# Kernel tuning notes

Hardware: AMD Instinct MI355X
Metric: run time of the kernel (lower is better)

The kernel has to match this reference:

```python
import jax, jax.numpy as jnp
import numpy as np

NUM_FUTURE = 4  # num_future_time_steps module constant


def _wmean(x, src, dst, ew, n):
    # Weighted mean aggregation over incoming edges (PyG SAGEConv aggr='mean'
    # with edge-weighted messages). x: [N,F] or [T,N,F].
    if x.ndim == 2:
        msg = x[src] * ew[:, None]                          # [E,F]
        agg = jax.ops.segment_sum(msg, dst, num_segments=n)  # [N,F]
    else:
        msg = x[:, src, :] * ew[None, :, None]              # [T,E,F]
        agg = jax.ops.segment_sum(jnp.moveaxis(msg, 1, 0), dst, num_segments=n)
        agg = jnp.moveaxis(agg, 0, 1)                       # [T,N,F]
    deg = jax.ops.segment_sum(jnp.ones_like(ew), dst, num_segments=n)
    return agg / jnp.clip(deg, 1.0)[:, None]


def _sage(x, src, dst, ew, Wr, Wroot, b, n):
    # WeightedSAGEConv: lin_rel(weighted-mean of neighbors) + lin_root(x)
    return _wmean(x, src, dst, ew, n) @ Wr + x @ Wroot + b


def _glstm(xseq, src, dst, ew, Wr, Wroot, b, h0, c0, n):
    # Graph LSTM: all four gates are WeightedSAGEConv([x_t, h]) ; the gate
    # convs share one gather/scatter (linear in agg), weights stacked to 4H.
    def step(carry, xt):
        h, c = carry
        inp = jnp.concatenate([xt, h], axis=-1)             # [N,2H]
        gates = _wmean(inp, src, dst, ew, n) @ Wr + inp @ Wroot + b  # [N,4H]
        i, f, g, o = jnp.split(gates, 4, axis=-1)
        c = jax.nn.sigmoid(f) * c + jax.nn.sigmoid(i) * jnp.tanh(g)
        h = jax.nn.sigmoid(o) * jnp.tanh(c)
        return (h, c), h
    (h, c), hs = jax.lax.scan(step, (h0, c0), xseq)
    return hs, c  # hs: [T,N,H]


def setup_inputs():
    T, N, E = 12, 20000, 400000
    F, H, O = 32, 64, 8
    key = jax.random.key(0)
    ks = jax.random.split(key, 12)
    nrm = lambda k, shp, fan: jax.random.normal(k, shp, dtype=jnp.float32) / np.float32(np.sqrt(fan))
    return {
        "x": jax.random.normal(ks[0], (T, N, F), dtype=jnp.float32),
        "edge_index": jax.random.randint(ks[1], (2, E), 0, N, dtype=jnp.int32),
        "edge_attr": jax.random.uniform(ks[2], (E,), dtype=jnp.float32),
        "sage_Wr": nrm(ks[3], (F, H), F),
        "sage_Wroot": nrm(ks[4], (F, H), F),
        "sage_b": jnp.zeros((H,), jnp.float32),
        "lstm1_Wr": nrm(ks[5], (2 * H, 4 * H), 2 * H),
        "lstm1_Wroot": nrm(ks[6], (2 * H, 4 * H), 2 * H),
        "lstm1_b": jnp.zeros((4 * H,), jnp.float32),
        "lstm2_Wr": nrm(ks[7], (2 * H, 4 * H), 2 * H),
        "lstm2_Wroot": nrm(ks[8], (2 * H, 4 * H), 2 * H),
        "lstm2_b": jnp.zeros((4 * H,), jnp.float32),
        "W_out": nrm(ks[9], (2 * H, O), 2 * H),
        "b_out": jnp.zeros((O,), jnp.float32),
    }


def reference(x, edge_index, edge_attr, sage_Wr, sage_Wroot, sage_b,
              lstm1_Wr, lstm1_Wroot, lstm1_b, lstm2_Wr, lstm2_Wroot, lstm2_b,
              W_out, b_out):
    src, dst = edge_index[0], edge_index[1]
    N = x.shape[1]
    H = sage_Wr.shape[1]
    emb = _sage(x, src, dst, edge_attr, sage_Wr, sage_Wroot, sage_b, N)  # [T,N,H]
    xr = jax.nn.relu(emb)  # dropout = identity (eval mode)
    h0 = jnp.zeros((N, H), x.dtype)
    c0 = jnp.zeros((N, H), x.dtype)
    h1, c1 = _glstm(xr, src, dst, edge_attr, lstm1_Wr, lstm1_Wroot, lstm1_b, h0, c0, N)
    h2, c2 = _glstm(xr, src, dst, edge_attr, lstm2_Wr, lstm2_Wroot, lstm2_b, h1[-1], c1, N)
    xs = jnp.concatenate([xr, h2], axis=-1)              # skip connection, [T,N,2H]
    out = xs[-NUM_FUTURE:] @ W_out + b_out               # [4,N,O]
    return out, c2, emb
```

## Files before the change

### kernel.cpp

```cpp
#include <hip/hip_runtime.h>
#include <math.h>

#define TT 12
#define FF 32
#define HH 64
#define OO 8
#define GG 256
#define NF 4
#define BR 16

typedef __bf16 bf16x8 __attribute__((ext_vector_type(8)));
typedef float  f32x4  __attribute__((ext_vector_type(4)));

__device__ __forceinline__ float sigmoidf_(float x){ return 1.f/(1.f+expf(-x)); }
__device__ __forceinline__ unsigned short f2bf(float f){
  unsigned int u = __float_as_uint(f);
  u += 0x7FFFu + ((u >> 16) & 1u);
  return (unsigned short)(u >> 16);
}
__device__ __forceinline__ float bf2f(unsigned short b){
  return __uint_as_float(((unsigned int)b) << 16);
}

__global__ void hist_kernel(const int* __restrict__ dst, int* __restrict__ cnt, int E){
  int e = blockIdx.x*blockDim.x + threadIdx.x;
  if (e < E) atomicAdd(&cnt[dst[e]], 1);
}

__global__ __launch_bounds__(1024) void scan_kernel(const int* __restrict__ cnt,
                                                    int* __restrict__ ptr,
                                                    float* __restrict__ invd, int N){
  __shared__ int buf[1024];
  __shared__ int carry;
  if (threadIdx.x == 0) carry = 0;
  __syncthreads();
  for (int base = 0; base < N; base += 1024){
    int i = base + threadIdx.x;
    int v = (i < N) ? cnt[i] : 0;
    buf[threadIdx.x] = v;
    __syncthreads();
    for (int off = 1; off < 1024; off <<= 1){
      int t = (threadIdx.x >= off) ? buf[threadIdx.x - off] : 0;
      __syncthreads();
      buf[threadIdx.x] += t;
      __syncthreads();
    }
    int incl = buf[threadIdx.x];
    if (i < N){
      ptr[i] = carry + incl - v;
      invd[i] = 1.f / fmaxf((float)v, 1.f);
    }
    __syncthreads();
    if (threadIdx.x == 1023){
      carry += incl;
      if (base + 1024 >= N) ptr[N] = carry;
    }
    __syncthreads();
  }
}

__global__ void fill_kernel(const int* __restrict__ src, const int* __restrict__ dst,
                            const float* __restrict__ ew, const int* __restrict__ ptr,
                            int* __restrict__ fill, int2* __restrict__ csr_sw, int E){
  int e = blockIdx.x*blockDim.x + threadIdx.x;
  if (e >= E) return;
  int d = dst[e];
  int pos = ptr[d] + atomicAdd(&fill[d], 1);
  int2 m; m.x = src[e]; m.y = __float_as_int(ew[e]);
  csr_sw[pos] = m;
}

__global__ void xpose_conv(const float* __restrict__ in, unsigned short* __restrict__ out,
                           int N){
  int idx = blockIdx.x*blockDim.x + threadIdx.x;
  if (idx >= TT*N*FF) return;
  int f = idx & (FF-1);
  int rem = idx >> 5;
  int t = rem % TT, n = rem / TT;
  out[idx] = f2bf(in[(size_t)t*N*FF + (size_t)n*FF + f]);
}

__global__ void pack_wfrag(const float* __restrict__ Wr, const float* __restrict__ Wroot,
                           unsigned short* __restrict__ Wfrag){
  int idx = blockIdx.x*256 + threadIdx.x;
  if (idx >= 16*8*64*8) return;
  int e  = idx & 7;
  int l  = (idx >> 3) & 63;
  int ks = (idx >> 9) & 7;
  int jt = idx >> 12;
  int k = ks*32 + (l>>4)*8 + e;
  int j = jt*16 + (l&15);
  float v = (k < 128) ? Wr[(size_t)k*GG + j] : Wroot[(size_t)(k-128)*GG + j];
  Wfrag[idx] = f2bf(v);
}

__global__ void pack_sfrag(const float* __restrict__ Wr, const float* __restrict__ Wroot,
                           unsigned short* __restrict__ Sfrag){
  int idx = blockIdx.x*256 + threadIdx.x;
  if (idx >= 4*2*64*8) return;
  int e  = idx & 7;
  int l  = (idx >> 3) & 63;
  int ks = (idx >> 9) & 1;
  int jt = idx >> 10;
  int k = ks*32 + (l>>4)*8 + e;
  int j = jt*16 + (l&15);
  float v = (k < 32) ? Wr[(size_t)k*HH + j] : Wroot[(size_t)(k-32)*HH + j];
  Sfrag[idx] = f2bf(v);
}

__global__ __launch_bounds__(256) void sage_gather(
    const unsigned short* __restrict__ xb, const int* __restrict__ ptr,
    const int2* __restrict__ csr_sw,
    const float* __restrict__ invd, unsigned short* __restrict__ aggb, int N){
  int wave = threadIdx.x >> 6, lane = threadIdx.x & 63;
  int f = lane & 31, tp = lane >> 5;
  int n = blockIdx.x*4 + wave;
  if (n >= N) return;
  int beg = ptr[n], end = ptr[n+1];
  float id = invd[n];
  float acc[TT/2];
  #pragma unroll
  for (int th = 0; th < TT/2; ++th) acc[th] = 0.f;
  int e = beg;
  for (; e+2 <= end; e += 2){
    int2 m0 = csr_sw[e], m1 = csr_sw[e+1];
    const unsigned short* p0 = xb + (size_t)m0.x*TT*FF + tp*FF + f;
    const unsigned short* p1 = xb + (size_t)m1.x*TT*FF + tp*FF + f;
    float w0 = __int_as_float(m0.y), w1 = __int_as_float(m1.y);
    #pragma unroll
    for (int th = 0; th < TT/2; ++th)
      acc[th] += bf2f(p0[2*th*FF])*w0 + bf2f(p1[2*th*FF])*w1;
  }
  for (; e < end; ++e){
    int2 m = csr_sw[e];
    const unsigned short* p = xb + (size_t)m.x*TT*FF + tp*FF + f;
    float wv = __int_as_float(m.y);
    #pragma unroll
    for (int th = 0; th < TT/2; ++th)
      acc[th] += bf2f(p[2*th*FF])*wv;
  }
  #pragma unroll
  for (int th = 0; th < TT/2; ++th)
    aggb[(size_t)n*TT*FF + (2*th+tp)*FF + f] = f2bf(acc[th] * id);
}

__global__ __launch_bounds__(256) void sage_mfma(
    const unsigned short* __restrict__ aggb, const unsigned short* __restrict__ xb,
    const unsigned short* __restrict__ Sfrag, const float* __restrict__ bias,
    float* __restrict__ emb, unsigned short* __restrict__ xrb, int N, int Mrows){
  int tid = threadIdx.x, wave = tid >> 6, lane = tid & 63;
  int rbase = blockIdx.x*64 + wave*16;
  if (rbase >= Mrows) return;
  int l15 = lane & 15, l4 = lane >> 4;
  int row = rbase + l15;
  bf16x8 af0 = *(const bf16x8*)&aggb[(size_t)row*FF + l4*8];
  bf16x8 af1 = *(const bf16x8*)&xb  [(size_t)row*FF + l4*8];
  f32x4 acc[4];
  #pragma unroll
  for (int jt = 0; jt < 4; ++jt){
    float bv = bias[jt*16 + l15];
    acc[jt][0]=bv; acc[jt][1]=bv; acc[jt][2]=bv; acc[jt][3]=bv;
  }
  #pragma unroll
  for (int jt = 0; jt < 4; ++jt){
    bf16x8 b0 = *(const bf16x8*)&Sfrag[(size_t)(((jt*2+0)*64) + lane) * 8];
    bf16x8 b1 = *(const bf16x8*)&Sfrag[(size_t)(((jt*2+1)*64) + lane) * 8];
    acc[jt] = __builtin_amdgcn_mfma_f32_16x16x32_bf16(af0, b0, acc[jt], 0, 0, 0);
    acc[jt] = __builtin_amdgcn_mfma_f32_16x16x32_bf16(af1, b1, acc[jt], 0, 0, 0);
  }
  #pragma unroll
  for (int jt = 0; jt < 4; ++jt){
    int col = jt*16 + l15;
    #pragma unroll
    for (int i = 0; i < 4; ++i){
      int ro = rbase + l4*4 + i;
      int t = ro % TT, n = ro / TT;
      float v = acc[jt][i];
      emb[(size_t)t*N*HH + (size_t)n*HH + col] = v;
      xrb[(size_t)ro*HH + col] = f2bf(fmaxf(v, 0.f));
    }
  }
}

__global__ __launch_bounds__(256) void xr_gather(
    const unsigned short* __restrict__ xrb, const int* __restrict__ ptr,
    const int2* __restrict__ csr_sw,
    const float* __restrict__ invd, unsigned short* __restrict__ xr_aggb, int N){
  int wave = threadIdx.x >> 6, lane = threadIdx.x & 63;
  int n = blockIdx.x*4 + wave;
  if (n >= N) return;
  int beg = ptr[n], end = ptr[n+1];
  float id = invd[n];
  float acc[TT];
  #pragma unroll
  for (int t = 0; t < TT; ++t) acc[t] = 0.f;
  int e = beg;
  for (; e+2 <= end; e += 2){
    int2 m0 = csr_sw[e], m1 = csr_sw[e+1];
    const unsigned short* p0 = xrb + (size_t)m0.x*TT*HH + lane;
    const unsigned short* p1 = xrb + (size_t)m1.x*TT*HH + lane;
    float w0 = __int_as_float(m0.y), w1 = __int_as_float(m1.y);
    #pragma unroll
    for (int t = 0; t < TT; ++t)
      acc[t] += bf2f(p0[t*HH])*w0 + bf2f(p1[t*HH])*w1;
  }
  for (; e < end; ++e){
    int2 m = csr_sw[e];
    const unsigned short* p = xrb + (size_t)m.x*TT*HH + lane;
    float wv = __int_as_float(m.y);
    #pragma unroll
    for (int t = 0; t < TT; ++t)
      acc[t] += bf2f(p[t*HH])*wv;
  }
  #pragma unroll
  for (int t = 0; t < TT; ++t)
    xr_aggb[(size_t)n*TT*HH + t*HH + lane] = f2bf(acc[t] * id);
}

__global__ __launch_bounds__(1024) void lstm_mfma(
    const unsigned short* __restrict__ xrb_t, const unsigned short* __restrict__ xraggb_t,
    const unsigned short* __restrict__ h_prev, unsigned short* __restrict__ h_next,
    float* __restrict__ c, const float* __restrict__ invd,
    const int* __restrict__ ptr, const int2* __restrict__ csr_sw,
    const unsigned short* __restrict__ Wfrag, const float* __restrict__ bias,
    unsigned short* __restrict__ h2_store, int N){
  __shared__ __align__(16) unsigned short Albuf[BR][264];
  __shared__ float gbuf[BR][260];
  int tid = threadIdx.x, wave = tid >> 6, lane = tid & 63;
  int base = blockIdx.x * BR;
  int n = base + wave;

  if (n < N){
    float id = invd[n];
    int beg = ptr[n], end = ptr[n+1];
    float a0=0.f,a1=0.f,a2=0.f,a3=0.f,a4=0.f,a5=0.f,a6=0.f,a7=0.f;
    int e = beg;
    for (; e+8 <= end; e += 8){
      int2 m0=csr_sw[e+0], m1=csr_sw[e+1], m2=csr_sw[e+2], m3=csr_sw[e+3];
      int2 m4=csr_sw[e+4], m5=csr_sw[e+5], m6=csr_sw[e+6], m7=csr_sw[e+7];
      a0 += bf2f(h_prev[(size_t)m0.x*HH+lane])*__int_as_float(m0.y);
      a1 += bf2f(h_prev[(size_t)m1.x*HH+lane])*__int_as_float(m1.y);
      a2 += bf2f(h_prev[(size_t)m2.x*HH+lane])*__int_as_float(m2.y);
      a3 += bf2f(h_prev[(size_t)m3.x*HH+lane])*__int_as_float(m3.y);
      a4 += bf2f(h_prev[(size_t)m4.x*HH+lane])*__int_as_float(m4.y);
      a5 += bf2f(h_prev[(size_t)m5.x*HH+lane])*__int_as_float(m5.y);
      a6 += bf2f(h_prev[(size_t)m6.x*HH+lane])*__int_as_float(m6.y);
      a7 += bf2f(h_prev[(size_t)m7.x*HH+lane])*__int_as_float(m7.y);
    }
    for (; e < end; ++e){
      int2 m = csr_sw[e];
      a0 += bf2f(h_prev[(size_t)m.x*HH+lane])*__int_as_float(m.y);
    }
    float hag = (((a0+a1)+(a2+a3))+((a4+a5)+(a6+a7))) * id;
    Albuf[wave][    lane] = xraggb_t[(size_t)n*TT*HH + lane];
    Albuf[wave][ 64+lane] = f2bf(hag);
    Albuf[wave][128+lane] = xrb_t [(size_t)n*TT*HH + lane];
    Albuf[wave][192+lane] = h_prev[(size_t)n*HH + lane];
  } else {
    Albuf[wave][lane] = Albuf[wave][64+lane] = Albuf[wave][128+lane] = Albuf[wave][192+lane] = 0;
  }
  __syncthreads();

  int l15 = lane & 15, l4 = lane >> 4;
  int jt = wave;
  f32x4 acc;
  {
    float bv = bias[jt*16 + l15];
    acc[0]=bv; acc[1]=bv; acc[2]=bv; acc[3]=bv;
  }
  #pragma unroll
  for (int ks = 0; ks < 8; ++ks){
    bf16x8 af = *(const bf16x8*)&Albuf[l15][ks*32 + l4*8];
    bf16x8 bf = *(const bf16x8*)&Wfrag[(size_t)(((jt*8 + ks)*64) + lane) * 8];
    acc = __builtin_amdgcn_mfma_f32_16x16x32_bf16(af, bf, acc, 0, 0, 0);
  }
  {
    int col = jt*16 + l15;
    #pragma unroll
    for (int i = 0; i < 4; ++i)
      gbuf[l4*4 + i][col] = acc[i];
  }
  __syncthreads();

  if (n < N){
    int r = wave;
    float gi = gbuf[r][lane], gf = gbuf[r][64+lane], gg2 = gbuf[r][128+lane], go = gbuf[r][192+lane];
    float cn = sigmoidf_(gf)*c[(size_t)n*HH+lane] + sigmoidf_(gi)*tanhf(gg2);
    float hn = sigmoidf_(go)*tanhf(cn);
    c[(size_t)n*HH+lane] = cn;
    unsigned short hb = f2bf(hn);
    h_next[(size_t)n*HH+lane] = hb;
    if (h2_store) h2_store[(size_t)n*HH+lane] = hb;
  }
}

__global__ void out_gemm(const unsigned short* __restrict__ xrb, const unsigned short* __restrict__ h2s,
                         const float* __restrict__ Wout, const float* __restrict__ bout,
                         float* __restrict__ out, int N){
  int idx = blockIdx.x*blockDim.x + threadIdx.x;
  if (idx >= NF*N*OO) return;
  int o = idx & (OO-1);
  int row = idx >> 3;
  int tt = row / N, n = row % N;
  const unsigned short* xv = xrb + ((size_t)n*TT + (TT-NF) + tt)*HH;
  const unsigned short* hv = h2s + (size_t)row*HH;
  float acc = bout[o];
  #pragma unroll
  for (int k = 0; k < HH; ++k)
    acc += bf2f(xv[k])*Wout[k*OO+o] + bf2f(hv[k])*Wout[(HH+k)*OO+o];
  out[idx] = acc;
}

__global__ void copyk(const float* __restrict__ s, float* __restrict__ d, int n){
  int i = blockIdx.x*blockDim.x + threadIdx.x;
  if (i < n) d[i] = s[i];
}

extern "C" void kernel_launch(void* const* d_in, const int* in_sizes, int n_in,
                              void* d_out, int out_size, void* d_ws, size_t ws_size,
                              hipStream_t stream){
  const float* x      = (const float*)d_in[0];
  const int*   ei     = (const int*)  d_in[1];
  const float* ew     = (const float*)d_in[2];
  const float* sWr    = (const float*)d_in[3];
  const float* sWroot = (const float*)d_in[4];
  const float* sb     = (const float*)d_in[5];
  const float* l1Wr   = (const float*)d_in[6];
  const float* l1Wroot= (const float*)d_in[7];
  const float* l1b    = (const float*)d_in[8];
  const float* l2Wr   = (const float*)d_in[9];
  const float* l2Wroot= (const float*)d_in[10];
  const float* l2b    = (const float*)d_in[11];
  const float* Wout   = (const float*)d_in[12];
  const float* bout   = (const float*)d_in[13];

  const int E = in_sizes[2];
  const int N = in_sizes[0] / (TT*FF);
  const int* src = ei;
  const int* dst = ei + E;

  float* out0   = (float*)d_out;
  float* c2out  = out0 + (size_t)NF*N*OO;
  float* embout = c2out + (size_t)N*HH;

  float* w = (float*)d_ws;
  float* cbuf   = w;  w += (size_t)N*HH;
  float* invd   = w;  w += N;
  int*   cnt    = (int*)w;  w += N;
  int*   fill   = (int*)w;  w += N;
  int*   ptr    = (int*)w;  w += (N+2);
  int2*  csr_sw = (int2*)w; w += (size_t)2*E;
  unsigned short* Wf1 = (unsigned short*)w; w += (size_t)16*8*64*8/2;
  unsigned short* Wf2 = (unsigned short*)w; w += (size_t)16*8*64*8/2;
  unsigned short* Sfg = (unsigned short*)w; w += (size_t)4*2*64*8/2;
  unsigned short* xb     = (unsigned short*)w; w += (size_t)TT*N*FF/2;
  unsigned short* aggb   = (unsigned short*)w; w += (size_t)TT*N*FF/2;
  unsigned short* xrb    = (unsigned short*)w; w += (size_t)TT*N*HH/2;
  unsigned short* xraggb = (unsigned short*)w; w += (size_t)TT*N*HH/2;
  unsigned short* hA     = (unsigned short*)w; w += (size_t)N*HH/2;
  unsigned short* hB     = (unsigned short*)w; w += (size_t)N*HH/2;
  unsigned short* h2s    = (unsigned short*)w; w += (size_t)NF*N*HH/2;

  hipMemsetAsync(cnt,  0, (size_t)N*4, stream);
  hipMemsetAsync(fill, 0, (size_t)N*4, stream);
  hipMemsetAsync(hA,   0, (size_t)N*HH*2, stream);
  hipMemsetAsync(cbuf, 0, (size_t)N*HH*4, stream);

  hist_kernel<<<(E+255)/256, 256, 0, stream>>>(dst, cnt, E);
  scan_kernel<<<1, 1024, 0, stream>>>(cnt, ptr, invd, N);
  fill_kernel<<<(E+255)/256, 256, 0, stream>>>(src, dst, ew, ptr, fill, csr_sw, E);

  pack_wfrag<<<(16*8*64*8+255)/256, 256, 0, stream>>>(l1Wr, l1Wroot, Wf1);
  pack_wfrag<<<(16*8*64*8+255)/256, 256, 0, stream>>>(l2Wr, l2Wroot, Wf2);
  pack_sfrag<<<(4*2*64*8+255)/256, 256, 0, stream>>>(sWr, sWroot, Sfg);
  xpose_conv<<<((size_t)TT*N*FF+255)/256, 256, 0, stream>>>(x, xb, N);

  sage_gather<<<(N+3)/4, 256, 0, stream>>>(xb, ptr, csr_sw, invd, aggb, N);
  {
    int Mrows = TT*N;
    sage_mfma<<<(Mrows+63)/64, 256, 0, stream>>>(aggb, xb, Sfg, sb, embout, xrb, N, Mrows);
  }
  xr_gather<<<(N+3)/4, 256, 0, stream>>>(xrb, ptr, csr_sw, invd, xraggb, N);

  const int sBlocks = (N+BR-1)/BR;
  unsigned short* hp = hA; unsigned short* hn = hB;
  for (int t = 0; t < TT; ++t){
    lstm_mfma<<<sBlocks, 1024, 0, stream>>>(xrb + (size_t)t*HH, xraggb + (size_t)t*HH,
                                            hp, hn, cbuf, invd, ptr, csr_sw,
                                            Wf1, l1b, nullptr, N);
    unsigned short* tmp = hp; hp = hn; hn = tmp;
  }
  for (int t = 0; t < TT; ++t){
    unsigned short* store = (t >= TT-NF) ? (h2s + (size_t)(t-(TT-NF))*N*HH) : nullptr;
    lstm_mfma<<<sBlocks, 1024, 0, stream>>>(xrb + (size_t)t*HH, xraggb + (size_t)t*HH,
                                            hp, hn, cbuf, invd, ptr, csr_sw,
                                            Wf2, l2b, store, N);
    unsigned short* tmp = hp; hp = hn; hn = tmp;
  }

  out_gemm<<<((size_t)NF*N*OO+255)/256, 256, 0, stream>>>(xrb, h2s,
                                                          Wout, bout, out0, N);
  copyk<<<((size_t)N*HH+255)/256, 256, 0, stream>>>(cbuf, c2out, N*HH);
}
```

Baseline: 1.004 ms.

## Fuse all 24 graph-LSTM steps into one persistent cooperative kernel

Replaces the 24 per-timestep lstm_mfma launches with a single cooperative kernel that loops over both LSTM layers and uses grid.sync between steps. Each 256-thread block now owns 16 rows, so each wave gathers 4 rows and computes 4 MFMA column tiles. The final c2 write is folded into the last step, which removes the separate copy kernel. The aim is to cut per-launch overhead and the tail gaps between dependent launches. In exchange, fewer waves per row are available to hide gather latency, and the kernel relies on all 1250 blocks being co-resident. A fallback to the old per-step launches is kept for when occupancy is too low.

```diff
diff --git a/kernel.cpp b/kernel.cpp
--- a/kernel.cpp
+++ b/kernel.cpp
@@ -1,5 +1,8 @@
 #include <hip/hip_runtime.h>
+#include <hip/hip_cooperative_groups.h>
 #include <math.h>
+
+namespace cg = cooperative_groups;
 
 #define TT 12
 #define FF 32
@@ -217,6 +220,105 @@
     xr_aggb[(size_t)n*TT*HH + t*HH + lane] = f2bf(acc[t] * id);
 }
 
+__global__ __launch_bounds__(256, 5) void lstm_persist(
+    const unsigned short* __restrict__ xrb, const unsigned short* __restrict__ xraggb,
+    unsigned short* __restrict__ hA, unsigned short* __restrict__ hB,
+    float* __restrict__ c, float* __restrict__ c2out,
+    const float* __restrict__ invd, const int* __restrict__ ptr,
+    const int2* __restrict__ csr_sw,
+    const unsigned short* __restrict__ Wf1, const float* __restrict__ b1,
+    const unsigned short* __restrict__ Wf2, const float* __restrict__ b2,
+    unsigned short* __restrict__ h2s, int N){
+  cg::grid_group grid = cg::this_grid();
+  __shared__ __align__(16) unsigned short Albuf[BR][264];
+  __shared__ float gbuf[BR][260];
+  int tid = threadIdx.x, wave = tid >> 6, lane = tid & 63;
+  int base = blockIdx.x * BR;
+  int l15 = lane & 15, l4 = lane >> 4;
+
+  unsigned short* hp = hA; unsigned short* hn = hB;
+  for (int s = 0; s < 2*TT; ++s){
+    const unsigned short* Wf = (s < TT) ? Wf1 : Wf2;
+    const float* bias        = (s < TT) ? b1  : b2;
+    int t = (s < TT) ? s : s - TT;
+
+    for (int r4 = 0; r4 < 4; ++r4){
+      int r = wave*4 + r4;
+      int n = base + r;
+      if (n < N){
+        float id = invd[n];
+        int beg = ptr[n], end = ptr[n+1];
+        float a0=0.f,a1=0.f,a2=0.f,a3=0.f,a4=0.f,a5=0.f,a6=0.f,a7=0.f;
+        int e = beg;
+        for (; e+8 <= end; e += 8){
+          int2 m0=csr_sw[e+0], m1=csr_sw[e+1], m2=csr_sw[e+2], m3=csr_sw[e+3];
+          int2 m4=csr_sw[e+4], m5=csr_sw[e+5], m6=csr_sw[e+6], m7=csr_sw[e+7];
+          a0 += bf2f(hp[(size_t)m0.x*HH+lane])*__int_as_float(m0.y);
+          a1 += bf2f(hp[(size_t)m1.x*HH+lane])*__int_as_float(m1.y);
+          a2 += bf2f(hp[(size_t)m2.x*HH+lane])*__int_as_float(m2.y);
+          a3 += bf2f(hp[(size_t)m3.x*HH+lane])*__int_as_float(m3.y);
+          a4 += bf2f(hp[(size_t)m4.x*HH+lane])*__int_as_float(m4.y);
+          a5 += bf2f(hp[(size_t)m5.x*HH+lane])*__int_as_float(m5.y);
+          a6 += bf2f(hp[(size_t)m6.x*HH+lane])*__int_as_float(m6.y);
+          a7 += bf2f(hp[(size_t)m7.x*HH+lane])*__int_as_float(m7.y);
+        }
+        for (; e < end; ++e){
+          int2 m = csr_sw[e];
+          a0 += bf2f(hp[(size_t)m.x*HH+lane])*__int_as_float(m.y);
+        }
+        float hag = (((a0+a1)+(a2+a3))+((a4+a5)+(a6+a7))) * id;
+        Albuf[r][    lane] = xraggb[((size_t)n*TT + t)*HH + lane];
+        Albuf[r][ 64+lane] = f2bf(hag);
+        Albuf[r][128+lane] = xrb   [((size_t)n*TT + t)*HH + lane];
+        Albuf[r][192+lane] = hp    [(size_t)n*HH + lane];
+      } else {
+        Albuf[r][lane] = Albuf[r][64+lane] = Albuf[r][128+lane] = Albuf[r][192+lane] = 0;
+      }
+    }
+    __syncthreads();
+
+    f32x4 acc[4];
+    #pragma unroll
+    for (int jtl = 0; jtl < 4; ++jtl){
+      float bv = bias[wave*64 + jtl*16 + l15];
+      acc[jtl][0]=bv; acc[jtl][1]=bv; acc[jtl][2]=bv; acc[jtl][3]=bv;
+    }
+    #pragma unroll
+    for (int ks = 0; ks < 8; ++ks){
+      bf16x8 af = *(const bf16x8*)&Albuf[l15][ks*32 + l4*8];
+      #pragma unroll
+      for (int jtl = 0; jtl < 4; ++jtl){
+        int jt = wave*4 + jtl;
+        bf16x8 bf = *(const bf16x8*)&Wf[(size_t)(((jt*8 + ks)*64) + lane) * 8];
+        acc[jtl] = __builtin_amdgcn_mfma_f32_16x16x32_bf16(af, bf, acc[jtl], 0, 0, 0);
+      }
+    }
+    #pragma unroll
+    for (int jtl = 0; jtl < 4; ++jtl){
+      int col = wave*64 + jtl*16 + l15;
+      #pragma unroll
+      for (int i = 0; i < 4; ++i)
+        gbuf[l4*4 + i][col] = acc[jtl][i];
+    }
+    __syncthreads();
+
+    for (int r = wave; r < BR; r += 4){
+      int n = base + r;
+      if (n >= N) continue;
+      float gi = gbuf[r][lane], gf = gbuf[r][64+lane], gg2 = gbuf[r][128+lane], go = gbuf[r][192+lane];
+      float cn = sigmoidf_(gf)*c[(size_t)n*HH+lane] + sigmoidf_(gi)*tanhf(gg2);
+      float hnv = sigmoidf_(go)*tanhf(cn);
+      c[(size_t)n*HH+lane] = cn;
+      unsigned short hb = f2bf(hnv);
+      hn[(size_t)n*HH+lane] = hb;
+      if (s >= TT + (TT-NF)) h2s[(size_t)(s - TT - (TT-NF))*N*HH + (size_t)n*HH + lane] = hb;
+      if (s == 2*TT-1) c2out[(size_t)n*HH+lane] = cn;
+    }
+    grid.sync();
+    unsigned short* tmp = hp; hp = hn; hn = tmp;
+  }
+}
+
 __global__ __launch_bounds__(1024) void lstm_mfma(
     const unsigned short* __restrict__ xrb_t, const unsigned short* __restrict__ xraggb_t,
     const unsigned short* __restrict__ h_prev, unsigned short* __restrict__ h_next,
@@ -286,9 +388,9 @@
     int r = wave;
     float gi = gbuf[r][lane], gf = gbuf[r][64+lane], gg2 = gbuf[r][128+lane], go = gbuf[r][192+lane];
     float cn = sigmoidf_(gf)*c[(size_t)n*HH+lane] + sigmoidf_(gi)*tanhf(gg2);
-    float hn = sigmoidf_(go)*tanhf(cn);
+    float hnv = sigmoidf_(go)*tanhf(cn);
     c[(size_t)n*HH+lane] = cn;
-    unsigned short hb = f2bf(hn);
+    unsigned short hb = f2bf(hnv);
     h_next[(size_t)n*HH+lane] = hb;
     if (h2_store) h2_store[(size_t)n*HH+lane] = hb;
   }
@@ -382,23 +484,49 @@
   }
   xr_gather<<<(N+3)/4, 256, 0, stream>>>(xrb, ptr, csr_sw, invd, xraggb, N);
 
-  const int sBlocks = (N+BR-1)/BR;
-  unsigned short* hp = hA; unsigned short* hn = hB;
-  for (int t = 0; t < TT; ++t){
-    lstm_mfma<<<sBlocks, 1024, 0, stream>>>(xrb + (size_t)t*HH, xraggb + (size_t)t*HH,
-                                            hp, hn, cbuf, invd, ptr, csr_sw,
-                                            Wf1, l1b, nullptr, N);
-    unsigned short* tmp = hp; hp = hn; hn = tmp;
-  }
-  for (int t = 0; t < TT; ++t){
-    unsigned short* store = (t >= TT-NF) ? (h2s + (size_t)(t-(TT-NF))*N*HH) : nullptr;
-    lstm_mfma<<<sBlocks, 1024, 0, stream>>>(xrb + (size_t)t*HH, xraggb + (size_t)t*HH,
-                                            hp, hn, cbuf, invd, ptr, csr_sw,
-                                            Wf2, l2b, store, N);
-    unsigned short* tmp = hp; hp = hn; hn = tmp;
+  const int ntiles = (N + BR - 1) / BR;
+
+  int dev = 0; hipGetDevice(&dev);
+  int numCU = 0;
+  hipDeviceGetAttribute(&numCU, hipDeviceAttributeMultiprocessorCount, dev);
+  int maxBlkPerCU = 0;
+  hipError_t occErr = hipOccupancyMaxActiveBlocksPerMultiprocessor(
+      &maxBlkPerCU, (const void*)lstm_persist, 256, 0);
+  long capacity = (long)maxBlkPerCU * (long)numCU;
+  const bool usePersist = (occErr == hipSuccess) && (capacity >= ntiles);
+
+  if (usePersist){
+    const unsigned short* a_xrb = xrb; const unsigned short* a_xraggb = xraggb;
+    unsigned short* a_hA = hA; unsigned short* a_hB = hB;
+    float* a_c = cbuf; float* a_c2 = c2out;
+    const float* a_invd = invd; const int* a_ptr = ptr; const int2* a_csr = csr_sw;
+    const unsigned short* a_w1 = Wf1; const float* a_b1 = l1b;
+    const unsigned short* a_w2 = Wf2; const float* a_b2 = l2b;
+    unsigned short* a_h2s = h2s; int a_N = N;
+    void* args[] = { (void*)&a_xrb, (void*)&a_xraggb, (void*)&a_hA, (void*)&a_hB,
+                     (void*)&a_c, (void*)&a_c2, (void*)&a_invd, (void*)&a_ptr, (void*)&a_csr,
+                     (void*)&a_w1, (void*)&a_b1, (void*)&a_w2, (void*)&a_b2,
+                     (void*)&a_h2s, (void*)&a_N };
+    hipLaunchCooperativeKernel((const void*)lstm_persist, dim3(ntiles), dim3(256),
+                               args, 0, stream);
+  } else {
+    unsigned short* hp = hA; unsigned short* hn = hB;
+    for (int t = 0; t < TT; ++t){
+      lstm_mfma<<<ntiles, 1024, 0, stream>>>(xrb + (size_t)t*HH, xraggb + (size_t)t*HH,
+                                             hp, hn, cbuf, invd, ptr, csr_sw,
+                                             Wf1, l1b, nullptr, N);
+      unsigned short* tmp = hp; hp = hn; hn = tmp;
+    }
+    for (int t = 0; t < TT; ++t){
+      unsigned short* store = (t >= TT-NF) ? (h2s + (size_t)(t-(TT-NF))*N*HH) : nullptr;
+      lstm_mfma<<<ntiles, 1024, 0, stream>>>(xrb + (size_t)t*HH, xraggb + (size_t)t*HH,
+                                             hp, hn, cbuf, invd, ptr, csr_sw,
+                                             Wf2, l2b, store, N);
+      unsigned short* tmp = hp; hp = hn; hn = tmp;
+    }
+    copyk<<<((size_t)N*HH+255)/256, 256, 0, stream>>>(cbuf, c2out, N*HH);
   }
 
   out_gemm<<<((size_t)NF*N*OO+255)/256, 256, 0, stream>>>(xrb, h2s,
                                                           Wout, bout, out0, N);
-  copyk<<<((size_t)N*HH+255)/256, 256, 0, stream>>>(cbuf, c2out, N*HH);
-}
+}
```

Measured after the change: 1.005 ms. About the same (+0.1%).

## Process 32 rows per LSTM block so each weight fragment feeds two MFMAs

Applied to the files above, without the earlier changes.

Each 1024-thread LSTM step block now handles 32 nodes instead of 16. Each wave gathers neighbor aggregates for two nodes, and in the gate GEMM it loads each weight fragment once and uses it for two MFMA tiles. This halves the number of blocks and the weight-fragment global loads per row. In exchange each wave runs its gather sequentially over two nodes, which lengthens per-wave latency, and the block count drops to about 625, which may reduce parallelism on the device.

```diff
diff --git a/kernel.cpp b/kernel.cpp
--- a/kernel.cpp
+++ b/kernel.cpp
@@ -7,7 +7,7 @@
 #define OO 8
 #define GG 256
 #define NF 4
-#define BR 16
+#define BRS 32
 
 typedef __bf16 bf16x8 __attribute__((ext_vector_type(8)));
 typedef float  f32x4  __attribute__((ext_vector_type(4)));
@@ -224,73 +224,86 @@
     const int* __restrict__ ptr, const int2* __restrict__ csr_sw,
     const unsigned short* __restrict__ Wfrag, const float* __restrict__ bias,
     unsigned short* __restrict__ h2_store, int N){
-  __shared__ __align__(16) unsigned short Albuf[BR][264];
-  __shared__ float gbuf[BR][260];
+  __shared__ __align__(16) unsigned short Albuf[BRS][264];
+  __shared__ float gbuf[BRS][260];
   int tid = threadIdx.x, wave = tid >> 6, lane = tid & 63;
-  int base = blockIdx.x * BR;
-  int n = base + wave;
-
-  if (n < N){
-    float id = invd[n];
-    int beg = ptr[n], end = ptr[n+1];
-    float a0=0.f,a1=0.f,a2=0.f,a3=0.f,a4=0.f,a5=0.f,a6=0.f,a7=0.f;
-    int e = beg;
-    for (; e+8 <= end; e += 8){
-      int2 m0=csr_sw[e+0], m1=csr_sw[e+1], m2=csr_sw[e+2], m3=csr_sw[e+3];
-      int2 m4=csr_sw[e+4], m5=csr_sw[e+5], m6=csr_sw[e+6], m7=csr_sw[e+7];
-      a0 += bf2f(h_prev[(size_t)m0.x*HH+lane])*__int_as_float(m0.y);
-      a1 += bf2f(h_prev[(size_t)m1.x*HH+lane])*__int_as_float(m1.y);
-      a2 += bf2f(h_prev[(size_t)m2.x*HH+lane])*__int_as_float(m2.y);
-      a3 += bf2f(h_prev[(size_t)m3.x*HH+lane])*__int_as_float(m3.y);
-      a4 += bf2f(h_prev[(size_t)m4.x*HH+lane])*__int_as_float(m4.y);
-      a5 += bf2f(h_prev[(size_t)m5.x*HH+lane])*__int_as_float(m5.y);
-      a6 += bf2f(h_prev[(size_t)m6.x*HH+lane])*__int_as_float(m6.y);
-      a7 += bf2f(h_prev[(size_t)m7.x*HH+lane])*__int_as_float(m7.y);
-    }
-    for (; e < end; ++e){
-      int2 m = csr_sw[e];
-      a0 += bf2f(h_prev[(size_t)m.x*HH+lane])*__int_as_float(m.y);
-    }
-    float hag = (((a0+a1)+(a2+a3))+((a4+a5)+(a6+a7))) * id;
-    Albuf[wave][    lane] = xraggb_t[(size_t)n*TT*HH + lane];
-    Albuf[wave][ 64+lane] = f2bf(hag);
-    Albuf[wave][128+lane] = xrb_t [(size_t)n*TT*HH + lane];
-    Albuf[wave][192+lane] = h_prev[(size_t)n*HH + lane];
-  } else {
-    Albuf[wave][lane] = Albuf[wave][64+lane] = Albuf[wave][128+lane] = Albuf[wave][192+lane] = 0;
+  int base = blockIdx.x * BRS;
+
+  #pragma unroll
+  for (int r2 = 0; r2 < 2; ++r2){
+    int r = wave*2 + r2;
+    int n = base + r;
+    if (n < N){
+      float id = invd[n];
+      int beg = ptr[n], end = ptr[n+1];
+      float a0=0.f,a1=0.f,a2=0.f,a3=0.f,a4=0.f,a5=0.f,a6=0.f,a7=0.f;
+      int e = beg;
+      for (; e+8 <= end; e += 8){
+        int2 m0=csr_sw[e+0], m1=csr_sw[e+1], m2=csr_sw[e+2], m3=csr_sw[e+3];
+        int2 m4=csr_sw[e+4], m5=csr_sw[e+5], m6=csr_sw[e+6], m7=csr_sw[e+7];
+        a0 += bf2f(h_prev[(size_t)m0.x*HH+lane])*__int_as_float(m0.y);
+        a1 += bf2f(h_prev[(size_t)m1.x*HH+lane])*__int_as_float(m1.y);
+        a2 += bf2f(h_prev[(size_t)m2.x*HH+lane])*__int_as_float(m2.y);
+        a3 += bf2f(h_prev[(size_t)m3.x*HH+lane])*__int_as_float(m3.y);
+        a4 += bf2f(h_prev[(size_t)m4.x*HH+lane])*__int_as_float(m4.y);
+        a5 += bf2f(h_prev[(size_t)m5.x*HH+lane])*__int_as_float(m5.y);
+        a6 += bf2f(h_prev[(size_t)m6.x*HH+lane])*__int_as_float(m6.y);
+        a7 += bf2f(h_prev[(size_t)m7.x*HH+lane])*__int_as_float(m7.y);
+      }
+      for (; e < end; ++e){
+        int2 m = csr_sw[e];
+        a0 += bf2f(h_prev[(size_t)m.x*HH+lane])*__int_as_float(m.y);
+      }
+      float hag = (((a0+a1)+(a2+a3))+((a4+a5)+(a6+a7))) * id;
+      Albuf[r][    lane] = xraggb_t[(size_t)n*TT*HH + lane];
+      Albuf[r][ 64+lane] = f2bf(hag);
+      Albuf[r][128+lane] = xrb_t [(size_t)n*TT*HH + lane];
+      Albuf[r][192+lane] = h_prev[(size_t)n*HH + lane];
+    } else {
+      Albuf[r][lane] = Albuf[r][64+lane] = Albuf[r][128+lane] = Albuf[r][192+lane] = 0;
+    }
   }
   __syncthreads();
 
   int l15 = lane & 15, l4 = lane >> 4;
   int jt = wave;
-  f32x4 acc;
+  f32x4 acc0, acc1;
   {
     float bv = bias[jt*16 + l15];
-    acc[0]=bv; acc[1]=bv; acc[2]=bv; acc[3]=bv;
+    acc0[0]=bv; acc0[1]=bv; acc0[2]=bv; acc0[3]=bv;
+    acc1 = acc0;
   }
   #pragma unroll
   for (int ks = 0; ks < 8; ++ks){
-    bf16x8 af = *(const bf16x8*)&Albuf[l15][ks*32 + l4*8];
-    bf16x8 bf = *(const bf16x8*)&Wfrag[(size_t)(((jt*8 + ks)*64) + lane) * 8];
-    acc = __builtin_amdgcn_mfma_f32_16x16x32_bf16(af, bf, acc, 0, 0, 0);
+    bf16x8 bfr = *(const bf16x8*)&Wfrag[(size_t)(((jt*8 + ks)*64) + lane) * 8];
+    bf16x8 af0 = *(const bf16x8*)&Albuf[l15     ][ks*32 + l4*8];
+    bf16x8 af1 = *(const bf16x8*)&Albuf[16 + l15][ks*32 + l4*8];
+    acc0 = __builtin_amdgcn_mfma_f32_16x16x32_bf16(af0, bfr, acc0, 0, 0, 0);
+    acc1 = __builtin_amdgcn_mfma_f32_16x16x32_bf16(af1, bfr, acc1, 0, 0, 0);
   }
   {
     int col = jt*16 + l15;
     #pragma unroll
-    for (int i = 0; i < 4; ++i)
-      gbuf[l4*4 + i][col] = acc[i];
+    for (int i = 0; i < 4; ++i){
+      gbuf[     l4*4 + i][col] = acc0[i];
+      gbuf[16 + l4*4 + i][col] = acc1[i];
+    }
   }
   __syncthreads();
 
-  if (n < N){
-    int r = wave;
-    float gi = gbuf[r][lane], gf = gbuf[r][64+lane], gg2 = gbuf[r][128+lane], go = gbuf[r][192+lane];
-    float cn = sigmoidf_(gf)*c[(size_t)n*HH+lane] + sigmoidf_(gi)*tanhf(gg2);
-    float hn = sigmoidf_(go)*tanhf(cn);
-    c[(size_t)n*HH+lane] = cn;
-    unsigned short hb = f2bf(hn);
-    h_next[(size_t)n*HH+lane] = hb;
-    if (h2_store) h2_store[(size_t)n*HH+lane] = hb;
+  #pragma unroll
+  for (int r2 = 0; r2 < 2; ++r2){
+    int r = wave*2 + r2;
+    int n = base + r;
+    if (n < N){
+      float gi = gbuf[r][lane], gf = gbuf[r][64+lane], gg2 = gbuf[r][128+lane], go = gbuf[r][192+lane];
+      float cn = sigmoidf_(gf)*c[(size_t)n*HH+lane] + sigmoidf_(gi)*tanhf(gg2);
+      float hnv = sigmoidf_(go)*tanhf(cn);
+      c[(size_t)n*HH+lane] = cn;
+      unsigned short hb = f2bf(hnv);
+      h_next[(size_t)n*HH+lane] = hb;
+      if (h2_store) h2_store[(size_t)n*HH+lane] = hb;
+    }
   }
 }
 
@@ -382,7 +395,7 @@
   }
   xr_gather<<<(N+3)/4, 256, 0, stream>>>(xrb, ptr, csr_sw, invd, xraggb, N);
 
-  const int sBlocks = (N+BR-1)/BR;
+  const int sBlocks = (N + BRS - 1) / BRS;
   unsigned short* hp = hA; unsigned short* hn = hB;
   for (int t = 0; t < TT; ++t){
     lstm_mfma<<<sBlocks, 1024, 0, stream>>>(xrb + (size_t)t*HH, xraggb + (size_t)t*HH,
```

Result: slower. 1.064 ms (+5.9%).

## Parallelize CSR degree scan across blocks and skip zero-h gather at first LSTM step

Applied to the files above, without the earlier changes.

Replaces the single-block serial prefix scan over node degrees with a three-kernel multi-block scan (local block scans, a single-wave scan of block totals, and a fixup pass). The first layer-1 LSTM step now skips the neighbor gather of h, because h0 is zero, and writes zeros directly, which also removes the memset of the initial h buffer. The multi-block scan adds two extra kernel launches, and scan_tot handles at most 64 blocks, which limits N to 65536.

```diff
diff --git a/kernel.cpp b/kernel.cpp
--- a/kernel.cpp
+++ b/kernel.cpp
@@ -27,36 +27,46 @@
   if (e < E) atomicAdd(&cnt[dst[e]], 1);
 }
 
-__global__ __launch_bounds__(1024) void scan_kernel(const int* __restrict__ cnt,
-                                                    int* __restrict__ ptr,
-                                                    float* __restrict__ invd, int N){
+__global__ __launch_bounds__(1024) void scan_local(const int* __restrict__ cnt,
+                                                   int* __restrict__ loc,
+                                                   int* __restrict__ btot, int N){
   __shared__ int buf[1024];
-  __shared__ int carry;
-  if (threadIdx.x == 0) carry = 0;
+  int i = blockIdx.x*1024 + threadIdx.x;
+  int v = (i < N) ? cnt[i] : 0;
+  buf[threadIdx.x] = v;
   __syncthreads();
-  for (int base = 0; base < N; base += 1024){
-    int i = base + threadIdx.x;
-    int v = (i < N) ? cnt[i] : 0;
-    buf[threadIdx.x] = v;
+  for (int off = 1; off < 1024; off <<= 1){
+    int t = (threadIdx.x >= off) ? buf[threadIdx.x - off] : 0;
     __syncthreads();
-    for (int off = 1; off < 1024; off <<= 1){
-      int t = (threadIdx.x >= off) ? buf[threadIdx.x - off] : 0;
-      __syncthreads();
-      buf[threadIdx.x] += t;
-      __syncthreads();
-    }
-    int incl = buf[threadIdx.x];
-    if (i < N){
-      ptr[i] = carry + incl - v;
-      invd[i] = 1.f / fmaxf((float)v, 1.f);
-    }
+    buf[threadIdx.x] += t;
     __syncthreads();
-    if (threadIdx.x == 1023){
-      carry += incl;
-      if (base + 1024 >= N) ptr[N] = carry;
-    }
-    __syncthreads();
-  }
+  }
+  if (i < N) loc[i] = buf[threadIdx.x] - v;
+  if (threadIdx.x == 1023) btot[blockIdx.x] = buf[1023];
+}
+
+__global__ void scan_tot(const int* __restrict__ btot, int* __restrict__ boff,
+                         int nb, int* __restrict__ ptrN){
+  int l = threadIdx.x;
+  int v = (l < nb) ? btot[l] : 0;
+  int incl = v;
+  for (int off = 1; off < 64; off <<= 1){
+    int t = __shfl_up(incl, off);
+    if (l >= off) incl += t;
+  }
+  if (l < nb) boff[l] = incl - v;
+  if (l == nb-1) *ptrN = incl;
+}
+
+__global__ __launch_bounds__(1024) void scan_fix(const int* __restrict__ loc,
+                                                 const int* __restrict__ boff,
+                                                 const int* __restrict__ cnt,
+                                                 int* __restrict__ ptr,
+                                                 float* __restrict__ invd, int N){
+  int i = blockIdx.x*1024 + threadIdx.x;
+  if (i >= N) return;
+  ptr[i]  = loc[i] + boff[blockIdx.x];
+  invd[i] = 1.f / fmaxf((float)cnt[i], 1.f);
 }
 
 __global__ void fill_kernel(const int* __restrict__ src, const int* __restrict__ dst,
@@ -223,7 +233,7 @@
     float* __restrict__ c, const float* __restrict__ invd,
     const int* __restrict__ ptr, const int2* __restrict__ csr_sw,
     const unsigned short* __restrict__ Wfrag, const float* __restrict__ bias,
-    unsigned short* __restrict__ h2_store, int N){
+    unsigned short* __restrict__ h2_store, int N, int skip_h){
   __shared__ __align__(16) unsigned short Albuf[BR][264];
   __shared__ float gbuf[BR][260];
   int tid = threadIdx.x, wave = tid >> 6, lane = tid & 63;
@@ -231,31 +241,38 @@
   int n = base + wave;
 
   if (n < N){
-    float id = invd[n];
-    int beg = ptr[n], end = ptr[n+1];
-    float a0=0.f,a1=0.f,a2=0.f,a3=0.f,a4=0.f,a5=0.f,a6=0.f,a7=0.f;
-    int e = beg;
-    for (; e+8 <= end; e += 8){
-      int2 m0=csr_sw[e+0], m1=csr_sw[e+1], m2=csr_sw[e+2], m3=csr_sw[e+3];
-      int2 m4=csr_sw[e+4], m5=csr_sw[e+5], m6=csr_sw[e+6], m7=csr_sw[e+7];
-      a0 += bf2f(h_prev[(size_t)m0.x*HH+lane])*__int_as_float(m0.y);
-      a1 += bf2f(h_prev[(size_t)m1.x*HH+lane])*__int_as_float(m1.y);
-      a2 += bf2f(h_prev[(size_t)m2.x*HH+lane])*__int_as_float(m2.y);
-      a3 += bf2f(h_prev[(size_t)m3.x*HH+lane])*__int_as_float(m3.y);
-      a4 += bf2f(h_prev[(size_t)m4.x*HH+lane])*__int_as_float(m4.y);
-      a5 += bf2f(h_prev[(size_t)m5.x*HH+lane])*__int_as_float(m5.y);
-      a6 += bf2f(h_prev[(size_t)m6.x*HH+lane])*__int_as_float(m6.y);
-      a7 += bf2f(h_prev[(size_t)m7.x*HH+lane])*__int_as_float(m7.y);
+    if (skip_h){
+      Albuf[wave][    lane] = xraggb_t[(size_t)n*TT*HH + lane];
+      Albuf[wave][ 64+lane] = 0;
+      Albuf[wave][128+lane] = xrb_t [(size_t)n*TT*HH + lane];
+      Albuf[wave][192+lane] = 0;
+    } else {
+      float id = invd[n];
+      int beg = ptr[n], end = ptr[n+1];
+      float a0=0.f,a1=0.f,a2=0.f,a3=0.f,a4=0.f,a5=0.f,a6=0.f,a7=0.f;
+      int e = beg;
+      for (; e+8 <= end; e += 8){
+        int2 m0=csr_sw[e+0], m1=csr_sw[e+1], m2=csr_sw[e+2], m3=csr_sw[e+3];
+        int2 m4=csr_sw[e+4], m5=csr_sw[e+5], m6=csr_sw[e+6], m7=csr_sw[e+7];
+        a0 += bf2f(h_prev[(size_t)m0.x*HH+lane])*__int_as_float(m0.y);
+        a1 += bf2f(h_prev[(size_t)m1.x*HH+lane])*__int_as_float(m1.y);
+        a2 += bf2f(h_prev[(size_t)m2.x*HH+lane])*__int_as_float(m2.y);
+        a3 += bf2f(h_prev[(size_t)m3.x*HH+lane])*__int_as_float(m3.y);
+        a4 += bf2f(h_prev[(size_t)m4.x*HH+lane])*__int_as_float(m4.y);
+        a5 += bf2f(h_prev[(size_t)m5.x*HH+lane])*__int_as_float(m5.y);
+        a6 += bf2f(h_prev[(size_t)m6.x*HH+lane])*__int_as_float(m6.y);
+        a7 += bf2f(h_prev[(size_t)m7.x*HH+lane])*__int_as_float(m7.y);
+      }
+      for (; e < end; ++e){
+        int2 m = csr_sw[e];
+        a0 += bf2f(h_prev[(size_t)m.x*HH+lane])*__int_as_float(m.y);
+      }
+      float hag = (((a0+a1)+(a2+a3))+((a4+a5)+(a6+a7))) * id;
+      Albuf[wave][    lane] = xraggb_t[(size_t)n*TT*HH + lane];
+      Albuf[wave][ 64+lane] = f2bf(hag);
+      Albuf[wave][128+lane] = xrb_t [(size_t)n*TT*HH + lane];
+      Albuf[wave][192+lane] = h_prev[(size_t)n*HH + lane];
     }
-    for (; e < end; ++e){
-      int2 m = csr_sw[e];
-      a0 += bf2f(h_prev[(size_t)m.x*HH+lane])*__int_as_float(m.y);
-    }
-    float hag = (((a0+a1)+(a2+a3))+((a4+a5)+(a6+a7))) * id;
-    Albuf[wave][    lane] = xraggb_t[(size_t)n*TT*HH + lane];
-    Albuf[wave][ 64+lane] = f2bf(hag);
-    Albuf[wave][128+lane] = xrb_t [(size_t)n*TT*HH + lane];
-    Albuf[wave][192+lane] = h_prev[(size_t)n*HH + lane];
   } else {
     Albuf[wave][lane] = Albuf[wave][64+lane] = Albuf[wave][128+lane] = Albuf[wave][192+lane] = 0;
   }
@@ -286,9 +303,9 @@
     int r = wave;
     float gi = gbuf[r][lane], gf = gbuf[r][64+lane], gg2 = gbuf[r][128+lane], go = gbuf[r][192+lane];
     float cn = sigmoidf_(gf)*c[(size_t)n*HH+lane] + sigmoidf_(gi)*tanhf(gg2);
-    float hn = sigmoidf_(go)*tanhf(cn);
+    float hnv = sigmoidf_(go)*tanhf(cn);
     c[(size_t)n*HH+lane] = cn;
-    unsigned short hb = f2bf(hn);
+    unsigned short hb = f2bf(hnv);
     h_next[(size_t)n*HH+lane] = hb;
     if (h2_store) h2_store[(size_t)n*HH+lane] = hb;
   }
@@ -348,6 +365,9 @@
   float* invd   = w;  w += N;
   int*   cnt    = (int*)w;  w += N;
   int*   fill   = (int*)w;  w += N;
+  int*   loc    = (int*)w;  w += N;
+  int*   btot   = (int*)w;  w += 64;
+  int*   boff   = (int*)w;  w += 64;
   int*   ptr    = (int*)w;  w += (N+2);
   int2*  csr_sw = (int2*)w; w += (size_t)2*E;
   unsigned short* Wf1 = (unsigned short*)w; w += (size_t)16*8*64*8/2;
@@ -363,11 +383,13 @@
 
   hipMemsetAsync(cnt,  0, (size_t)N*4, stream);
   hipMemsetAsync(fill, 0, (size_t)N*4, stream);
-  hipMemsetAsync(hA,   0, (size_t)N*HH*2, stream);
   hipMemsetAsync(cbuf, 0, (size_t)N*HH*4, stream);
 
+  const int nb = (N + 1023) / 1024;
   hist_kernel<<<(E+255)/256, 256, 0, stream>>>(dst, cnt, E);
-  scan_kernel<<<1, 1024, 0, stream>>>(cnt, ptr, invd, N);
+  scan_local<<<nb, 1024, 0, stream>>>(cnt, loc, btot, N);
+  scan_tot<<<1, 64, 0, stream>>>(btot, boff, nb, ptr + N);
+  scan_fix<<<nb, 1024, 0, stream>>>(loc, boff, cnt, ptr, invd, N);
   fill_kernel<<<(E+255)/256, 256, 0, stream>>>(src, dst, ew, ptr, fill, csr_sw, E);
 
   pack_wfrag<<<(16*8*64*8+255)/256, 256, 0, stream>>>(l1Wr, l1Wroot, Wf1);
@@ -382,19 +404,19 @@
   }
   xr_gather<<<(N+3)/4, 256, 0, stream>>>(xrb, ptr, csr_sw, invd, xraggb, N);
 
-  const int sBlocks = (N+BR-1)/BR;
+  const int sBlocks = (N + BR - 1) / BR;
   unsigned short* hp = hA; unsigned short* hn = hB;
   for (int t = 0; t < TT; ++t){
     lstm_mfma<<<sBlocks, 1024, 0, stream>>>(xrb + (size_t)t*HH, xraggb + (size_t)t*HH,
                                             hp, hn, cbuf, invd, ptr, csr_sw,
-                                            Wf1, l1b, nullptr, N);
+                                            Wf1, l1b, nullptr, N, t == 0 ? 1 : 0);
     unsigned short* tmp = hp; hp = hn; hn = tmp;
   }
   for (int t = 0; t < TT; ++t){
     unsigned short* store = (t >= TT-NF) ? (h2s + (size_t)(t-(TT-NF))*N*HH) : nullptr;
     lstm_mfma<<<sBlocks, 1024, 0, stream>>>(xrb + (size_t)t*HH, xraggb + (size_t)t*HH,
                                             hp, hn, cbuf, invd, ptr, csr_sw,
-                                            Wf2, l2b, store, N);
+                                            Wf2, l2b, store, N, 0);
     unsigned short* tmp = hp; hp = hn; hn = tmp;
   }
 
```

Result: faster. 960.6 us (-4.3%).
